# Optimization experiments

Measured on AMD Instinct MI355X. Metric: run time of the kernel, lower is better.

The kernel has to match this reference:

```python
import jax, jax.numpy as jnp
import numpy as np

N_QUERY, N_BACKGND, DIM = 2048, 8192, 32


def setup_inputs() -> dict:
    key = jax.random.key(0)
    k0, k1, k2, k3 = jax.random.split(key, 4)
    x_backgnd = jax.random.normal(k0, (N_BACKGND, DIM), dtype=jnp.float32)
    y_backgnd = jax.random.normal(k1, (N_BACKGND,), dtype=jnp.float32)
    x_query = jax.random.normal(k2, (N_QUERY, DIM), dtype=jnp.float32)
    r = jax.random.uniform(k3, (N_QUERY, N_BACKGND), dtype=jnp.float32)
    sigma = jnp.array([0.1], dtype=jnp.float32)      # nn.Parameter init_sigma
    r_scale = jnp.array([3.0], dtype=jnp.float32)    # nn.Parameter init_r_scale
    w = jnp.ones((DIM,), dtype=jnp.float32)          # trainable weights matrix
    return {"x_backgnd": x_backgnd, "y_backgnd": y_backgnd, "x_query": x_query,
            "r": r, "sigma": sigma, "r_scale": r_scale, "w": w}


def reference(x_backgnd, y_backgnd, x_query, r, sigma, r_scale, w):
    # weighted Euclidean distance: ||(xq - xb) * w|| via the expansion trick,
    # avoiding the (n_query, n_backgnd, dim) difference tensor.
    xq = x_query * w           # (nq, d)
    xb = x_backgnd * w         # (nb, d)
    q2 = jnp.sum(xq * xq, axis=1, keepdims=True)        # (nq, 1)
    b2 = jnp.sum(xb * xb, axis=1)                        # (nb,)
    d2 = q2 + b2[None, :] - 2.0 * (xq @ xb.T)            # (nq, nb)
    dists = jnp.sqrt(jnp.maximum(d2, 0.0))
    # exp kernel with relationship bias, normalize, weighted sum
    k_vals = jnp.exp(-dists / sigma + r_scale * r)       # sigma, r_scale broadcast (1,)
    k_sum = jnp.sum(k_vals, axis=1, keepdims=True) + 1e-8
    weights = k_vals / k_sum
    y_pred = weights @ y_backgnd                          # (nq,)
    return y_pred
```

## Files before the change

### kernel.cpp

```cpp
#include <hip/hip_runtime.h>
#include <math.h>

#define NQ 2048
#define NB 8192
#define DIM 32

#define LOG2E 1.44269504088896340736f

typedef _Float16 half8 __attribute__((ext_vector_type(8)));
typedef float    f32x4 __attribute__((ext_vector_type(4)));

#define WS_ACC 0
#define WS_Q2  16448
#define WS_B2  24640
#define WS_XQH 57408
#define WS_XBH 188480

__global__ __launch_bounds__(256) void relnw_pre(
    const float* __restrict__ xq, const float* __restrict__ xb,
    const float* __restrict__ w,
    _Float16* __restrict__ XQh, _Float16* __restrict__ XBh,
    float* __restrict__ q2, float* __restrict__ b2,
    float* __restrict__ acc)
{
    const int tid = threadIdx.x;
    const int gi  = blockIdx.x * 256 + tid;
    if (gi < 2 * NQ) acc[gi] = 0.f;

    const int row = blockIdx.x * 64 + (tid >> 2);
    const int p   = tid & 3;
    if (row >= NQ + NB) return;

    const float* src; _Float16* dst; float* s2; float scale;
    if (row < NQ) { src = xq + (size_t)row * DIM;
                    dst = XQh + (size_t)row * DIM; s2 = q2 + row; scale = 1.f; }
    else          { int j = row - NQ;
                    src = xb + (size_t)j * DIM;
                    dst = XBh + (size_t)j * DIM;   s2 = b2 + j;   scale = -2.f; }

    const float4 xa  = ((const float4*)src)[p * 2];
    const float4 xbv = ((const float4*)src)[p * 2 + 1];
    const float4 wa  = ((const float4*)w)[p * 2];
    const float4 wb  = ((const float4*)w)[p * 2 + 1];
    const float xs[8]  = {xa.x, xa.y, xa.z, xa.w, xbv.x, xbv.y, xbv.z, xbv.w};
    const float ws_[8] = {wa.x, wa.y, wa.z, wa.w, wb.x, wb.y, wb.z, wb.w};

    half8 h;
    float s = 0.f;
#pragma unroll
    for (int c = 0; c < 8; ++c) {
        float t = xs[c] * ws_[c];
        _Float16 hh = (_Float16)t;
        float th = (float)hh;
        s = fmaf(th, th, s);
        h[c] = (_Float16)(th * scale);
    }
    *(half8*)(dst + p * 8) = h;

    s += __shfl_xor(s, 1, 64);
    s += __shfl_xor(s, 2, 64);
    if (p == 0) *s2 = s;
}

#define BT_PER_WAVE 16
#define BG_PER_WAVE (BT_PER_WAVE * 16)

#define GLDS(GSRC, LDST)                                                    \
  __builtin_amdgcn_global_load_lds(                                         \
      (const __attribute__((address_space(1))) void*)(GSRC),                \
      (__attribute__((address_space(3))) void*)(LDST), 16, 0, 0)

#define WAIT_VM0                                                            \
  { asm volatile("s_waitcnt vmcnt(0)" ::: "memory");                        \
    __builtin_amdgcn_sched_barrier(0); }
#define WAIT_LGKM0                                                          \
  { asm volatile("s_waitcnt lgkmcnt(0)" ::: "memory");                      \
    __builtin_amdgcn_sched_barrier(0); }

__global__ __launch_bounds__(256, 2) void relnw_main(
    const _Float16* __restrict__ XQh,
    const _Float16* __restrict__ XBh,
    const float* __restrict__ q2,
    const float* __restrict__ b2,
    const float* __restrict__ yb,
    const float* __restrict__ r,
    const float* __restrict__ sigma,
    const float* __restrict__ rscale,
    float* __restrict__ acc)
{
    __shared__ char lds[4 * 8192 + 4 * 1024 + 4 * 1024];

    const int tid  = threadIdx.x;
    const int lane = tid & 63;
    const int wid  = tid >> 6;
    const int m    = lane & 15;
    const int quad = lane >> 4;

    const int q0     = blockIdx.y * 16;
    const int bstart = (blockIdx.x * 4 + wid) * BG_PER_WAVE;

    char*  waveR = lds + wid * 8192;
    float* b2l   = (float*)(lds + 32768 + wid * 1024);
    float* ybl   = (float*)(lds + 36864 + wid * 1024);

    const float c1 = -LOG2E / sigma[0];
    const float c2 =  LOG2E * rscale[0];

    const half8 qfrag = *(const half8*)(XQh + (size_t)(q0 + m) * DIM + quad * 8);
    const float q2s   = q2[q0 + m];
    const int   swz   = (m & 7) << 4;

    GLDS((const char*)(b2 + bstart) + lane * 16, b2l);
    GLDS((const char*)(yb + bstart) + lane * 16, ybl);

    const int jj = lane >> 5;
    const int cc = lane & 31;
    const char* rsrc[8];
#pragma unroll
    for (int j = 0; j < 8; ++j) {
        const int rw = 2 * j + jj;
        rsrc[j] = (const char*)(r + (size_t)(q0 + rw) * NB + bstart)
                  + ((cc * 16) ^ ((rw & 7) << 4));
    }

#pragma unroll
    for (int j = 0; j < 8; ++j) GLDS(rsrc[j], waveR + j * 1024);

    half8 af[8];
#pragma unroll
    for (int i = 0; i < 8; ++i)
        af[i] = *(const half8*)(XBh + (size_t)(bstart + i * 16 + m) * DIM + quad * 8);

    float sk = 0.f, sky = 0.f;

    WAIT_VM0

#pragma unroll
    for (int h = 0; h < 2; ++h) {
        if (h == 1) {
#pragma unroll
            for (int i = 0; i < 8; ++i)
                af[i] = *(const half8*)(XBh +
                        (size_t)(bstart + 128 + i * 16 + m) * DIM + quad * 8);
            WAIT_LGKM0
#pragma unroll
            for (int j = 0; j < 8; ++j) GLDS(rsrc[j] + 512, waveR + j * 1024);
            WAIT_VM0
        }

#pragma unroll
        for (int it = 0; it < 8; ++it) {
            const int co = h * 128 + it * 16 + quad * 4;
            const f32x4 bb = *(const f32x4*)(b2l + co);
            const f32x4 yv = *(const f32x4*)(ybl + co);
            const f32x4 rr = *(const f32x4*)(waveR + m * 512 +
                                 ((it * 64 + quad * 16) ^ swz));

            f32x4 cin;
#pragma unroll
            for (int g = 0; g < 4; ++g) cin[g] = q2s + bb[g];

            const f32x4 d2v = __builtin_amdgcn_mfma_f32_16x16x32_f16(
                af[it], qfrag, cin, 0, 0, 0);

#pragma unroll
            for (int g = 0; g < 4; ++g) {
                float d2   = fmaxf(d2v[g], 0.f);
                float dist = __builtin_amdgcn_sqrtf(d2);
                float e    = fmaf(dist, c1, rr[g] * c2);
                float k    = __builtin_amdgcn_exp2f(e);
                sk += k;
                sky = fmaf(k, yv[g], sky);
            }
        }
    }

    sk  += __shfl_xor(sk, 16, 64);
    sk  += __shfl_xor(sk, 32, 64);
    sky += __shfl_xor(sky, 16, 64);
    sky += __shfl_xor(sky, 32, 64);
    if (lane < 16) {
        atomicAdd(acc + (q0 + m),      sk);
        atomicAdd(acc + NQ + (q0 + m), sky);
    }
}

__global__ __launch_bounds__(256) void relnw_finalize(
    const float* __restrict__ acc, float* __restrict__ out)
{
    int q = blockIdx.x * 256 + threadIdx.x;
    if (q < NQ)
        out[q] = acc[NQ + q] / (acc[q] + 1e-8f);
}

extern "C" void kernel_launch(void* const* d_in, const int* in_sizes, int n_in,
                              void* d_out, int out_size, void* d_ws, size_t ws_size,
                              hipStream_t stream) {
    const float* xb     = (const float*)d_in[0];
    const float* yb     = (const float*)d_in[1];
    const float* xq     = (const float*)d_in[2];
    const float* r      = (const float*)d_in[3];
    const float* sigma  = (const float*)d_in[4];
    const float* rscale = (const float*)d_in[5];
    const float* w      = (const float*)d_in[6];
    float* out = (float*)d_out;

    char* ws = (char*)d_ws;
    float*    acc = (float*)(ws + WS_ACC);
    float*    q2  = (float*)(ws + WS_Q2);
    float*    b2  = (float*)(ws + WS_B2);
    _Float16* XQh = (_Float16*)(ws + WS_XQH);
    _Float16* XBh = (_Float16*)(ws + WS_XBH);

    relnw_pre<<<(NQ + NB) / 64, 256, 0, stream>>>(xq, xb, w, XQh, XBh, q2, b2, acc);

    dim3 grid(NB / (4 * BG_PER_WAVE), NQ / 16);
    relnw_main<<<grid, 256, 0, stream>>>(XQh, XBh, q2, b2, yb, r, sigma, rscale, acc);

    relnw_finalize<<<(NQ + 255) / 256, 256, 0, stream>>>(acc, out);
}
```

Before: 109.2 us.

## Double-buffer r tiles in LDS with quarter-step pipelined loads

Splits each wave's 256-column background chunk into four quarters and double-buffers the r tile in LDS across two 4 KB buffers. Loads for the next quarter (r via global_load_lds and XB fragments into registers) are issued before computing the current one, with partial vmcnt waits instead of full drains. The goal is to overlap global memory latency with the MFMA and exp work rather than stalling between two halves. The cost is more live fragment registers and fragile hand-counted vmcnt values that must match the exact order in which loads are issued.

```diff
diff --git a/kernel.cpp b/kernel.cpp
--- a/kernel.cpp
+++ b/kernel.cpp
@@ -70,12 +70,26 @@
       (const __attribute__((address_space(1))) void*)(GSRC),                \
       (__attribute__((address_space(3))) void*)(LDST), 16, 0, 0)
 
-#define WAIT_VM0                                                            \
-  { asm volatile("s_waitcnt vmcnt(0)" ::: "memory");                        \
-    __builtin_amdgcn_sched_barrier(0); }
-#define WAIT_LGKM0                                                          \
-  { asm volatile("s_waitcnt lgkmcnt(0)" ::: "memory");                      \
-    __builtin_amdgcn_sched_barrier(0); }
+#define SBAR __builtin_amdgcn_sched_barrier(0)
+
+#define COMPQ(BUF, QTR, AF)                                                 \
+  { _Pragma("unroll") for (int it = 0; it < 4; ++it) {                      \
+      const int co = (QTR) * 64 + it * 16 + quad * 4;                       \
+      const f32x4 bb = *(const f32x4*)(b2l + co);                           \
+      const f32x4 yv = *(const f32x4*)(ybl + co);                           \
+      const f32x4 rr = *(const f32x4*)((BUF) + m * 256 +                    \
+                           ((it * 64 + quad * 16) ^ swz));                  \
+      f32x4 cin;                                                            \
+      _Pragma("unroll") for (int g = 0; g < 4; ++g) cin[g] = q2s + bb[g];   \
+      const f32x4 d2v = __builtin_amdgcn_mfma_f32_16x16x32_f16(             \
+          AF[it], qfrag, cin, 0, 0, 0);                                     \
+      _Pragma("unroll") for (int g = 0; g < 4; ++g) {                       \
+        float d2   = fmaxf(d2v[g], 0.f);                                    \
+        float dist = __builtin_amdgcn_sqrtf(d2);                            \
+        float e    = fmaf(dist, c1, rr[g] * c2);                            \
+        float k    = __builtin_amdgcn_exp2f(e);                             \
+        sk += k;                                                            \
+        sky = fmaf(k, yv[g], sky); } } }
 
 __global__ __launch_bounds__(256, 2) void relnw_main(
     const _Float16* __restrict__ XQh,
@@ -99,9 +113,10 @@
     const int q0     = blockIdx.y * 16;
     const int bstart = (blockIdx.x * 4 + wid) * BG_PER_WAVE;
 
-    char*  waveR = lds + wid * 8192;
-    float* b2l   = (float*)(lds + 32768 + wid * 1024);
-    float* ybl   = (float*)(lds + 36864 + wid * 1024);
+    char*  bufA = lds + wid * 8192;
+    char*  bufB = bufA + 4096;
+    float* b2l  = (float*)(lds + 32768 + wid * 1024);
+    float* ybl  = (float*)(lds + 36864 + wid * 1024);
 
     const float c1 = -LOG2E / sigma[0];
     const float c2 =  LOG2E * rscale[0];
@@ -110,70 +125,62 @@
     const float q2s   = q2[q0 + m];
     const int   swz   = (m & 7) << 4;
 
+    const int g16 = lane >> 4;
+    const int l16 = lane & 15;
+    const char* rsrc[4];
+#pragma unroll
+    for (int j = 0; j < 4; ++j) {
+        const int rw = 4 * j + g16;
+        rsrc[j] = (const char*)(r + (size_t)(q0 + rw) * NB + bstart)
+                  + ((l16 * 16) ^ ((rw & 7) << 4));
+    }
+
+#define AFRAG(I) (*(const half8*)(XBh + \
+        (size_t)(bstart + (I) * 16 + m) * DIM + quad * 8))
+
+    half8 afA[4], afB[4], afC[4], afD[4];
+    float sk = 0.f, sky = 0.f;
+
+#pragma unroll
+    for (int i = 0; i < 4; ++i) afA[i] = AFRAG(i);
+#pragma unroll
+    for (int i = 0; i < 4; ++i) afB[i] = AFRAG(4 + i);
     GLDS((const char*)(b2 + bstart) + lane * 16, b2l);
     GLDS((const char*)(yb + bstart) + lane * 16, ybl);
-
-    const int jj = lane >> 5;
-    const int cc = lane & 31;
-    const char* rsrc[8];
-#pragma unroll
-    for (int j = 0; j < 8; ++j) {
-        const int rw = 2 * j + jj;
-        rsrc[j] = (const char*)(r + (size_t)(q0 + rw) * NB + bstart)
-                  + ((cc * 16) ^ ((rw & 7) << 4));
-    }
-
-#pragma unroll
-    for (int j = 0; j < 8; ++j) GLDS(rsrc[j], waveR + j * 1024);
-
-    half8 af[8];
-#pragma unroll
-    for (int i = 0; i < 8; ++i)
-        af[i] = *(const half8*)(XBh + (size_t)(bstart + i * 16 + m) * DIM + quad * 8);
-
-    float sk = 0.f, sky = 0.f;
-
-    WAIT_VM0
-
-#pragma unroll
-    for (int h = 0; h < 2; ++h) {
-        if (h == 1) {
-#pragma unroll
-            for (int i = 0; i < 8; ++i)
-                af[i] = *(const half8*)(XBh +
-                        (size_t)(bstart + 128 + i * 16 + m) * DIM + quad * 8);
-            WAIT_LGKM0
-#pragma unroll
-            for (int j = 0; j < 8; ++j) GLDS(rsrc[j] + 512, waveR + j * 1024);
-            WAIT_VM0
-        }
-
-#pragma unroll
-        for (int it = 0; it < 8; ++it) {
-            const int co = h * 128 + it * 16 + quad * 4;
-            const f32x4 bb = *(const f32x4*)(b2l + co);
-            const f32x4 yv = *(const f32x4*)(ybl + co);
-            const f32x4 rr = *(const f32x4*)(waveR + m * 512 +
-                                 ((it * 64 + quad * 16) ^ swz));
-
-            f32x4 cin;
-#pragma unroll
-            for (int g = 0; g < 4; ++g) cin[g] = q2s + bb[g];
-
-            const f32x4 d2v = __builtin_amdgcn_mfma_f32_16x16x32_f16(
-                af[it], qfrag, cin, 0, 0, 0);
-
-#pragma unroll
-            for (int g = 0; g < 4; ++g) {
-                float d2   = fmaxf(d2v[g], 0.f);
-                float dist = __builtin_amdgcn_sqrtf(d2);
-                float e    = fmaf(dist, c1, rr[g] * c2);
-                float k    = __builtin_amdgcn_exp2f(e);
-                sk += k;
-                sky = fmaf(k, yv[g], sky);
-            }
-        }
-    }
+#pragma unroll
+    for (int j = 0; j < 4; ++j) GLDS(rsrc[j],       bufA + j * 1024);
+#pragma unroll
+    for (int j = 0; j < 4; ++j) GLDS(rsrc[j] + 256, bufB + j * 1024);
+    SBAR;
+    asm volatile("s_waitcnt vmcnt(4)" ::: "memory");
+    SBAR;
+
+    COMPQ(bufA, 0, afA)
+
+#pragma unroll
+    for (int i = 0; i < 4; ++i) afC[i] = AFRAG(8 + i);
+#pragma unroll
+    for (int i = 0; i < 4; ++i) afD[i] = AFRAG(12 + i);
+#pragma unroll
+    for (int j = 0; j < 4; ++j) GLDS(rsrc[j] + 512, bufA + j * 1024);
+    SBAR;
+    asm volatile("s_waitcnt vmcnt(12)" ::: "memory");
+    SBAR;
+
+    COMPQ(bufB, 1, afB)
+
+#pragma unroll
+    for (int j = 0; j < 4; ++j) GLDS(rsrc[j] + 768, bufB + j * 1024);
+    SBAR;
+    asm volatile("s_waitcnt vmcnt(4)" ::: "memory");
+    SBAR;
+
+    COMPQ(bufA, 2, afC)
+
+    asm volatile("s_waitcnt vmcnt(0)" ::: "memory");
+    SBAR;
+
+    COMPQ(bufB, 3, afD)
 
     sk  += __shfl_xor(sk, 16, 64);
     sk  += __shfl_xor(sk, 32, 64);
```

Measured after the change: 111.3 us. No clear change (+1.9%).
